# Kernel optimization log

Hardware: AMD Instinct MI355X
Metric: run time of the kernel (lower is better)

The kernel has to match this reference:

```python
import jax, jax.numpy as jnp
import numpy as np

N_NODES = 100000
N_EDGES = 1600000
IN_F, HID_F, OUT_F = 64, 64, 16


def setup_inputs() -> dict:
    key = jax.random.key(0)
    k_x, k_e, k_w1, k_w2 = jax.random.split(key, 4)
    x = jax.random.normal(k_x, (N_NODES, IN_F), dtype=jnp.float32)
    edge_index = jax.random.randint(k_e, (2, N_EDGES), 0, N_NODES, dtype=jnp.int64)
    # Glorot-ish init for the GCNConv linear weights; bias zeros (PyG default)
    W1 = jax.random.normal(k_w1, (IN_F, HID_F), dtype=jnp.float32) / np.sqrt(IN_F)
    b1 = jnp.zeros((HID_F,), dtype=jnp.float32)
    W2 = jax.random.normal(k_w2, (HID_F, OUT_F), dtype=jnp.float32) / np.sqrt(HID_F)
    b2 = jnp.zeros((OUT_F,), dtype=jnp.float32)
    return {"x": x, "edge_index": edge_index, "W1": W1, "b1": b1, "W2": W2, "b2": b2}


def reference(x, edge_index, W1, b1, W2, b2):
    N = x.shape[0]
    # GCNConv: add self-loops, symmetric normalization D^-1/2 A D^-1/2
    loop = jnp.arange(N, dtype=edge_index.dtype)
    src = jnp.concatenate([edge_index[0], loop])  # [E+N]
    dst = jnp.concatenate([edge_index[1], loop])  # [E+N]
    deg = jax.ops.segment_sum(jnp.ones_like(dst, dtype=x.dtype), dst, num_segments=N)
    dis = jax.lax.rsqrt(deg)  # deg >= 1 due to self-loops
    norm = dis[src] * dis[dst]  # [E+N]

    def gcn_conv(h, W, b):
        h = h @ W                                   # [N, d_out]
        msg = h[src] * norm[:, None]                # gather + scale  [E+N, d_out]
        agg = jax.ops.segment_sum(msg, dst, num_segments=N)  # scatter-add
        return agg + b

    h = jax.nn.relu(gcn_conv(x, W1, b1))
    h = gcn_conv(h, W2, b2)
    return jax.nn.log_softmax(h, axis=1)
```

## Files before the change

kernel.cpp:

```cpp
#include <hip/hip_runtime.h>
#include <hip/hip_bf16.h>
#include <hip/hip_fp16.h>


#define F1 64
#define F2 16
#define NBKT 256
#define BSH 512
#define NPB 256
#define SBD 1024
#define STG 9216

typedef _Float16 f16x8 __attribute__((ext_vector_type(8)));
typedef _Float16 f16x4 __attribute__((ext_vector_type(4)));
typedef float f32x2 __attribute__((ext_vector_type(2)));
typedef float f32x4 __attribute__((ext_vector_type(4)));
typedef float f32x8 __attribute__((ext_vector_type(8)));

__device__ inline f32x8 shfl_xor_f32x8(f32x8 v, int off) {
  f32x8 r;
#pragma unroll
  for (int k = 0; k < 8; ++k) r[k] = __shfl_xor(v[k], off);
  return r;
}
__device__ inline f32x4 shfl_xor_f32x4(f32x4 v, int off) {
  f32x4 r;
#pragma unroll
  for (int k = 0; k < 4; ++k) r[k] = __shfl_xor(v[k], off);
  return r;
}

__device__ inline void acc_fp8x8(f32x2* a, uint2 v) {
  a[0] += __builtin_amdgcn_cvt_pk_f32_fp8((int)v.x, false);
  a[1] += __builtin_amdgcn_cvt_pk_f32_fp8((int)v.x, true);
  a[2] += __builtin_amdgcn_cvt_pk_f32_fp8((int)v.y, false);
  a[3] += __builtin_amdgcn_cvt_pk_f32_fp8((int)v.y, true);
}

__global__ void k_w(const float* __restrict__ W1, const float* __restrict__ W2,
                    const float* __restrict__ b1,
                    __half* __restrict__ W1T, __half* __restrict__ W2Tp,
                    float* __restrict__ b1p, int* __restrict__ bcur, int nb) {
  int t = threadIdx.x;
  for (int i = t; i < 64 * 64; i += 256) {
    int n = i >> 6, k = i & 63;
    W1T[i] = __float2half(W1[k * 64 + n]);
  }
  for (int i = t; i < 16 * 64; i += 256) {
    int j = i >> 6, p = i & 63;
    int fp = 16 * (p & 3) + (p >> 2);
    W2Tp[i] = __float2half(W2[fp * 16 + j]);
  }
  if (t < 64) b1p[t] = b1[16 * (t & 3) + (t >> 2)];
  if (t < nb) bcur[t] = t * STG;
}

__global__ void k_bscatter(const int* __restrict__ src, const int* __restrict__ dst,
                           int* __restrict__ bcur, int* __restrict__ tmp,
                           int E, int nb, int chunk) {
  __shared__ int h[NBKT];
  __shared__ int cur[NBKT];
  int t = threadIdx.x, sb = blockIdx.x;
  int beg = sb * chunk, end = min(beg + chunk, E);
  if (t < NBKT) h[t] = 0;
  __syncthreads();
  int e;
  for (e = beg + t * 4; e + 4 <= end; e += 4 * SBD) {
    int4 d4 = *(const int4*)(dst + e);
    atomicAdd(&h[d4.x >> 9], 1);
    atomicAdd(&h[d4.y >> 9], 1);
    atomicAdd(&h[d4.z >> 9], 1);
    atomicAdd(&h[d4.w >> 9], 1);
  }
  for (; e < end; ++e) atomicAdd(&h[dst[e] >> 9], 1);
  __syncthreads();
  if (t < nb) cur[t] = atomicAdd(&bcur[t], h[t]);
  __syncthreads();
  for (e = beg + t * 4; e + 4 <= end; e += 4 * SBD) {
    int4 d4 = *(const int4*)(dst + e);
    int4 s4 = *(const int4*)(src + e);
    int b, off;
    b = d4.x >> 9; off = atomicAdd(&cur[b], 1); tmp[off] = (s4.x << 9) | (d4.x & 511);
    b = d4.y >> 9; off = atomicAdd(&cur[b], 1); tmp[off] = (s4.y << 9) | (d4.y & 511);
    b = d4.z >> 9; off = atomicAdd(&cur[b], 1); tmp[off] = (s4.z << 9) | (d4.z & 511);
    b = d4.w >> 9; off = atomicAdd(&cur[b], 1); tmp[off] = (s4.w << 9) | (d4.w & 511);
  }
  for (; e < end; ++e) {
    int d = dst[e];
    int b = d >> 9;
    int off = atomicAdd(&cur[b], 1);
    tmp[off] = (src[e] << 9) | (d & 511);
  }
}

__global__ void k_csr(const int* __restrict__ tmp, const int* __restrict__ bcur,
                      int* __restrict__ csr, int* __restrict__ rowptr,
                      float* __restrict__ dis, int N, int nb) {
  __shared__ int stage[STG];
  __shared__ int sc[BSH];
  __shared__ int cnt[BSH];
  __shared__ int lofs[BSH];
  int b = blockIdx.x, t = threadIdx.x;
  int lenb = bcur[b] - b * STG;
  if (t < NBKT) sc[t] = (t < nb) ? (bcur[t] - t * STG) : 0;
  __syncthreads();
  for (int off = 1; off < NBKT; off <<= 1) {
    int a = (t < NBKT && t >= off) ? sc[t - off] : 0;
    __syncthreads();
    if (t < NBKT) sc[t] += a;
    __syncthreads();
  }
  int beg = (b == 0) ? 0 : sc[b - 1];
  __syncthreads();
  int s0 = b * STG;
  int lim = lenb & ~3;
  for (int i = t * 4; i < lim; i += 4 * BSH)
    *(int4*)(stage + i) = *(const int4*)(tmp + s0 + i);
  {
    int r = lim + t;
    if (r < lenb) stage[r] = tmp[s0 + r];
  }
  cnt[t] = 0;
  __syncthreads();
  for (int i = t; i < lenb; i += BSH) atomicAdd(&cnt[stage[i] & (BSH - 1)], 1);
  __syncthreads();
  sc[t] = cnt[t];
  __syncthreads();
  for (int off = 1; off < BSH; off <<= 1) {
    int a = (t >= off) ? sc[t - off] : 0;
    __syncthreads();
    sc[t] += a;
    __syncthreads();
  }
  int excl = (t == 0) ? 0 : sc[t - 1];
  lofs[t] = excl;
  int n = b * BSH + t;
  if (n <= N) rowptr[n] = beg + excl;
  if (n < N) dis[n] = rsqrtf((float)(cnt[t] + 1));
  cnt[t] = 0;
  __syncthreads();
  for (int i = t; i < lenb; i += BSH) {
    int p = stage[i];
    int l = p & (BSH - 1);
    int off = atomicAdd(&cnt[l], 1);
    csr[beg + lofs[l] + off] = p >> 9;
  }
}

__global__ void k_gemm1(const float* __restrict__ x, const __half* __restrict__ W1T,
                        const float* __restrict__ dis, unsigned char* __restrict__ out,
                        int N) {
  int t = threadIdx.x;
  int wv = t >> 6, lane = t & 63;
  int m = lane & 15, q = lane >> 4;
  int row0 = blockIdx.x * 64 + wv * 16;
  int arow = min(row0 + m, N - 1);
  const _Float16* wt = (const _Float16*)W1T;
  f16x8 bf[4][2];
#pragma unroll
  for (int c = 0; c < 4; ++c)
#pragma unroll
    for (int kt = 0; kt < 2; ++kt)
      bf[c][kt] = *(const f16x8*)&wt[(c * 16 + m) * 64 + kt * 32 + q * 8];
  f16x8 a[2];
#pragma unroll
  for (int kt = 0; kt < 2; ++kt) {
    const float4* xp = (const float4*)(x + (size_t)arow * 64 + kt * 32 + q * 8);
    float4 u = xp[0], v = xp[1];
    a[kt][0] = (_Float16)u.x; a[kt][1] = (_Float16)u.y;
    a[kt][2] = (_Float16)u.z; a[kt][3] = (_Float16)u.w;
    a[kt][4] = (_Float16)v.x; a[kt][5] = (_Float16)v.y;
    a[kt][6] = (_Float16)v.z; a[kt][7] = (_Float16)v.w;
  }
  f32x4 acc[4] = {};
#pragma unroll
  for (int kt = 0; kt < 2; ++kt)
#pragma unroll
    for (int c = 0; c < 4; ++c)
      acc[c] = __builtin_amdgcn_mfma_f32_16x16x32_f16(a[kt], bf[c][kt], acc[c], 0, 0, 0);
#pragma unroll
  for (int r = 0; r < 4; ++r) {
    int n = row0 + q * 4 + r;
    if (n < N) {
      float dn = dis[n];
      int d = __builtin_amdgcn_cvt_pk_fp8_f32(acc[0][r] * dn, acc[1][r] * dn, 0, false);
      d = __builtin_amdgcn_cvt_pk_fp8_f32(acc[2][r] * dn, acc[3][r] * dn, d, true);
      *(unsigned int*)(out + (size_t)n * 64 + m * 4) = (unsigned)d;
    }
  }
}

__global__ void k_agg1f(const unsigned char* __restrict__ h, const float* __restrict__ dis,
                        const int* __restrict__ rowptr, const int* __restrict__ csr,
                        const float* __restrict__ b1p, const __half* __restrict__ W2Tp,
                        __half* __restrict__ h2, int N) {
  int gt = blockIdx.x * blockDim.x + threadIdx.x;
  int w = gt >> 6;
  int lane = gt & 63;
  int half = lane >> 5;
  int sub = (lane >> 3) & 3;
  int fl = lane & 7;
  int n = w * 2 + half;
  if (n >= N) return;
  float dn = dis[n];
  float4 bu = *(const float4*)(b1p + fl * 8);
  float4 bv = *(const float4*)(b1p + fl * 8 + 4);
  const _Float16* wt = (const _Float16*)W2Tp;
  f16x8 wj[4];
#pragma unroll
  for (int i = 0; i < 4; ++i)
    wj[i] = *(const f16x8*)&wt[(sub * 4 + i) * 64 + fl * 8];
  f32x2 a0[4] = {}, a1[4] = {};
  if (sub == 0)
    acc_fp8x8(a0, *(const uint2*)&h[(size_t)n * 64 + fl * 8]);
  int beg = rowptr[n], end = rowptr[n + 1];
  int e = beg + sub;
  int sA = (e < end) ? csr[e] : -1;
  int sB = (e + 4 < end) ? csr[e + 4] : -1;
  while (sB >= 0) {
    int e2 = e + 8;
    int sC = (e2 < end) ? csr[e2] : -1;
    int sD = (e2 + 4 < end) ? csr[e2 + 4] : -1;
    uint2 v0 = *(const uint2*)&h[(size_t)sA * 64 + fl * 8];
    uint2 v1 = *(const uint2*)&h[(size_t)sB * 64 + fl * 8];
    acc_fp8x8(a0, v0);
    acc_fp8x8(a1, v1);
    sA = sC; sB = sD; e = e2;
  }
  if (sA >= 0)
    acc_fp8x8(a0, *(const uint2*)&h[(size_t)sA * 64 + fl * 8]);
  f32x8 acc;
#pragma unroll
  for (int k = 0; k < 4; ++k) {
    f32x2 s = a0[k] + a1[k];
    acc[2 * k] = s[0];
    acc[2 * k + 1] = s[1];
  }
  acc += shfl_xor_f32x8(acc, 8);
  acc += shfl_xor_f32x8(acc, 16);
  float bb[8] = {bu.x, bu.y, bu.z, bu.w, bv.x, bv.y, bv.z, bv.w};
  float hr[8];
#pragma unroll
  for (int k = 0; k < 8; ++k)
    hr[k] = fmaxf(fmaf(dn, acc[k], bb[k]), 0.f);
  float p[4];
#pragma unroll
  for (int i = 0; i < 4; ++i) {
    float s = 0.f;
#pragma unroll
    for (int k = 0; k < 8; ++k) s = fmaf(hr[k], (float)wj[i][k], s);
    s += __shfl_xor(s, 1);
    s += __shfl_xor(s, 2);
    s += __shfl_xor(s, 4);
    p[i] = s;
  }
  if (fl == 0) {
    f16x4 o;
#pragma unroll
    for (int i = 0; i < 4; ++i) o[i] = (_Float16)(p[i] * dn);
    *(f16x4*)((_Float16*)h2 + (size_t)n * 16 + sub * 4) = o;
  }
}

__global__ void k_agg2(const __half* __restrict__ h2, const float* __restrict__ dis,
                       const int* __restrict__ rowptr, const int* __restrict__ csr,
                       const float* __restrict__ b2, float* __restrict__ out, int N) {
  int gt = blockIdx.x * blockDim.x + threadIdx.x;
  int w = gt >> 6;
  int lane = gt & 63;
  int half = lane >> 5;
  int sub = (lane >> 2) & 7;
  int fl = lane & 3;
  int n = w * 2 + half;
  if (n >= N) return;
  const _Float16* hp = (const _Float16*)h2;
  f32x4 acc0 = {}, acc1 = {};
  if (sub == 0)
    acc0 = __builtin_convertvector(*(const f16x4*)&hp[(size_t)n * 16 + fl * 4], f32x4);
  int beg = rowptr[n], end = rowptr[n + 1];
  int e = beg + sub;
  int sA = (e < end) ? csr[e] : -1;
  int sB = (e + 8 < end) ? csr[e + 8] : -1;
  while (sB >= 0) {
    int e2 = e + 16;
    int sC = (e2 < end) ? csr[e2] : -1;
    int sD = (e2 + 8 < end) ? csr[e2 + 8] : -1;
    f16x4 v0 = *(const f16x4*)&hp[(size_t)sA * 16 + fl * 4];
    f16x4 v1 = *(const f16x4*)&hp[(size_t)sB * 16 + fl * 4];
    acc0 += __builtin_convertvector(v0, f32x4);
    acc1 += __builtin_convertvector(v1, f32x4);
    sA = sC; sB = sD; e = e2;
  }
  if (sA >= 0)
    acc0 += __builtin_convertvector(*(const f16x4*)&hp[(size_t)sA * 16 + fl * 4], f32x4);
  f32x4 acc = acc0 + acc1;
  acc += shfl_xor_f32x4(acc, 4);
  acc += shfl_xor_f32x4(acc, 8);
  acc += shfl_xor_f32x4(acc, 16);
  if (sub == 0) {
    float dn = dis[n];
    float4 bb = *(const float4*)(b2 + fl * 4);
    float v0 = fmaf(dn, acc[0], bb.x);
    float v1 = fmaf(dn, acc[1], bb.y);
    float v2 = fmaf(dn, acc[2], bb.z);
    float v3 = fmaf(dn, acc[3], bb.w);
    float m = fmaxf(fmaxf(v0, v1), fmaxf(v2, v3));
    m = fmaxf(m, __shfl_xor(m, 1));
    m = fmaxf(m, __shfl_xor(m, 2));
    float s2 = __expf(v0 - m) + __expf(v1 - m) + __expf(v2 - m) + __expf(v3 - m);
    s2 += __shfl_xor(s2, 1);
    s2 += __shfl_xor(s2, 2);
    float ls = m + __logf(s2);
    float4 o = {v0 - ls, v1 - ls, v2 - ls, v3 - ls};
    *(float4*)(out + (size_t)n * 16 + fl * 4) = o;
  }
}

extern "C" void kernel_launch(void* const* d_in, const int* in_sizes, int n_in,
                              void* d_out, int out_size, void* d_ws, size_t ws_size,
                              hipStream_t stream) {
  const float* x = (const float*)d_in[0];
  const int* ei = (const int*)d_in[1];
  const float* W1 = (const float*)d_in[2];
  const float* b1 = (const float*)d_in[3];
  const float* W2 = (const float*)d_in[4];
  const float* b2 = (const float*)d_in[5];
  float* out = (float*)d_out;

  int N = in_sizes[0] / F1;
  int E = in_sizes[1] / 2;
  const int* src = ei;
  const int* dst = ei + E;
  int nb = (N + BSH - 1) >> 9;
  int chunk = ((E + NPB - 1) / NPB + 3) & ~3;

  char* ws = (char*)d_ws;
  size_t o_w1t = 0;
  size_t o_w2t = o_w1t + 64 * 64 * 2;
  size_t o_b1p = (o_w2t + 16 * 64 * 2 + 255) & ~(size_t)255;
  size_t o_bcur = (o_b1p + 64 * 4 + 255) & ~(size_t)255;
  size_t o_dis = (o_bcur + NBKT * 4 + 255) & ~(size_t)255;
  size_t o_rowp = (o_dis + (size_t)N * 4 + 255) & ~(size_t)255;
  size_t o_tmp = (o_rowp + (size_t)(N + 1) * 4 + 255) & ~(size_t)255;
  size_t o_csr = (o_tmp + (size_t)nb * STG * 4 + 255) & ~(size_t)255;
  size_t o_h1 = (o_csr + (size_t)E * 4 + 255) & ~(size_t)255;
  size_t o_h2 = (o_h1 + (size_t)N * 64 + 255) & ~(size_t)255;

  __half* W1T = (__half*)(ws + o_w1t);
  __half* W2Tp = (__half*)(ws + o_w2t);
  float* b1p = (float*)(ws + o_b1p);
  int* bcur = (int*)(ws + o_bcur);
  float* dis = (float*)(ws + o_dis);
  int* rowptr = (int*)(ws + o_rowp);
  int* tmp = (int*)(ws + o_tmp);
  int* csr = (int*)(ws + o_csr);
  unsigned char* h1 = (unsigned char*)(ws + o_h1);
  __half* h2 = (__half*)(ws + o_h2);

  k_w<<<1, 256, 0, stream>>>(W1, W2, b1, W1T, W2Tp, b1p, bcur, nb);
  k_bscatter<<<NPB, SBD, 0, stream>>>(src, dst, bcur, tmp, E, nb, chunk);
  k_csr<<<nb, BSH, 0, stream>>>(tmp, bcur, csr, rowptr, dis, N, nb);
  int gb = (N + 63) / 64;
  k_gemm1<<<gb, 256, 0, stream>>>(x, W1T, dis, h1, N);
  int aw = (N + 1) / 2;
  k_agg1f<<<((size_t)aw * 64 + 255) / 256, 256, 0, stream>>>(h1, dis, rowptr, csr, b1p, W2Tp, h2, N);
  k_agg2<<<((size_t)aw * 64 + 255) / 256, 256, 0, stream>>>(h2, dis, rowptr, csr, b2, out, N);
}
```

Before: 184.3 us.

## Fuse weight prep into bscatter, merge CSR build with GEMM1, deepen aggregation prefetch

The weight transpose/convert kernel becomes an extra block of the bucket-scatter kernel, and bucket cursors plus a new per-node degree array are zeroed by a memset. Degrees are counted with global atomics during scatter, so GEMM1 no longer waits on the CSR build and runs as extra blocks of the same launch, computing dis itself. Merging kernels cuts launch count and lets the CSR build and GEMM1 run concurrently. The layer-1 aggregation loop now prefetches four neighbor indices instead of two to raise memory-level parallelism. The cost is 1.6M extra global atomics on deg, with contention on popular nodes.

Result: slower. 251.2 us (+36.4%).

```diff
diff --git a/kernel.cpp b/kernel.cpp
--- a/kernel.cpp
+++ b/kernel.cpp
@@ -37,30 +37,29 @@
   a[3] += __builtin_amdgcn_cvt_pk_f32_fp8((int)v.y, true);
 }
 
-__global__ void k_w(const float* __restrict__ W1, const float* __restrict__ W2,
-                    const float* __restrict__ b1,
-                    __half* __restrict__ W1T, __half* __restrict__ W2Tp,
-                    float* __restrict__ b1p, int* __restrict__ bcur, int nb) {
-  int t = threadIdx.x;
-  for (int i = t; i < 64 * 64; i += 256) {
-    int n = i >> 6, k = i & 63;
-    W1T[i] = __float2half(W1[k * 64 + n]);
-  }
-  for (int i = t; i < 16 * 64; i += 256) {
-    int j = i >> 6, p = i & 63;
-    int fp = 16 * (p & 3) + (p >> 2);
-    W2Tp[i] = __float2half(W2[fp * 16 + j]);
-  }
-  if (t < 64) b1p[t] = b1[16 * (t & 3) + (t >> 2)];
-  if (t < nb) bcur[t] = t * STG;
-}
-
 __global__ void k_bscatter(const int* __restrict__ src, const int* __restrict__ dst,
                            int* __restrict__ bcur, int* __restrict__ tmp,
-                           int E, int nb, int chunk) {
+                           int* __restrict__ deg, int E, int nb, int chunk,
+                           const float* __restrict__ W1, const float* __restrict__ W2,
+                           const float* __restrict__ b1,
+                           __half* __restrict__ W1T, __half* __restrict__ W2Tp,
+                           float* __restrict__ b1p) {
+  int t = threadIdx.x, sb = blockIdx.x;
+  if (sb == NPB) {
+    for (int i = t; i < 64 * 64; i += SBD) {
+      int n = i >> 6, k = i & 63;
+      W1T[i] = __float2half(W1[k * 64 + n]);
+    }
+    for (int i = t; i < 16 * 64; i += SBD) {
+      int j = i >> 6, p = i & 63;
+      int fp = 16 * (p & 3) + (p >> 2);
+      W2Tp[i] = __float2half(W2[fp * 16 + j]);
+    }
+    if (t < 64) b1p[t] = b1[16 * (t & 3) + (t >> 2)];
+    return;
+  }
   __shared__ int h[NBKT];
   __shared__ int cur[NBKT];
-  int t = threadIdx.x, sb = blockIdx.x;
   int beg = sb * chunk, end = min(beg + chunk, E);
   if (t < NBKT) h[t] = 0;
   __syncthreads();
@@ -71,10 +70,18 @@
     atomicAdd(&h[d4.y >> 9], 1);
     atomicAdd(&h[d4.z >> 9], 1);
     atomicAdd(&h[d4.w >> 9], 1);
-  }
-  for (; e < end; ++e) atomicAdd(&h[dst[e] >> 9], 1);
-  __syncthreads();
-  if (t < nb) cur[t] = atomicAdd(&bcur[t], h[t]);
+    atomicAdd(&deg[d4.x], 1);
+    atomicAdd(&deg[d4.y], 1);
+    atomicAdd(&deg[d4.z], 1);
+    atomicAdd(&deg[d4.w], 1);
+  }
+  for (; e < end; ++e) {
+    int d = dst[e];
+    atomicAdd(&h[d >> 9], 1);
+    atomicAdd(&deg[d], 1);
+  }
+  __syncthreads();
+  if (t < nb) cur[t] = t * STG + atomicAdd(&bcur[t], h[t]);
   __syncthreads();
   for (e = beg + t * 4; e + 4 <= end; e += 4 * SBD) {
     int4 d4 = *(const int4*)(dst + e);
@@ -93,16 +100,60 @@
   }
 }
 
-__global__ void k_csr(const int* __restrict__ tmp, const int* __restrict__ bcur,
-                      int* __restrict__ csr, int* __restrict__ rowptr,
-                      float* __restrict__ dis, int N, int nb) {
+__global__ void k_cg(const int* __restrict__ tmp, const int* __restrict__ bcur,
+                     int* __restrict__ csr, int* __restrict__ rowptr,
+                     const float* __restrict__ x, const __half* __restrict__ W1T,
+                     const int* __restrict__ deg, float* __restrict__ dis,
+                     unsigned char* __restrict__ h1, int N, int nb) {
   __shared__ int stage[STG];
   __shared__ int sc[BSH];
   __shared__ int cnt[BSH];
   __shared__ int lofs[BSH];
   int b = blockIdx.x, t = threadIdx.x;
-  int lenb = bcur[b] - b * STG;
-  if (t < NBKT) sc[t] = (t < nb) ? (bcur[t] - t * STG) : 0;
+  if (b >= nb) {
+    int g = b - nb;
+    int wv = t >> 6, lane = t & 63;
+    int m = lane & 15, q = lane >> 4;
+    int row0 = g * 128 + wv * 16;
+    int arow = min(row0 + m, N - 1);
+    const _Float16* wt = (const _Float16*)W1T;
+    f16x8 bf[4][2];
+#pragma unroll
+    for (int c = 0; c < 4; ++c)
+#pragma unroll
+      for (int kt = 0; kt < 2; ++kt)
+        bf[c][kt] = *(const f16x8*)&wt[(c * 16 + m) * 64 + kt * 32 + q * 8];
+    f16x8 a[2];
+#pragma unroll
+    for (int kt = 0; kt < 2; ++kt) {
+      const float4* xp = (const float4*)(x + (size_t)arow * 64 + kt * 32 + q * 8);
+      float4 u = xp[0], v = xp[1];
+      a[kt][0] = (_Float16)u.x; a[kt][1] = (_Float16)u.y;
+      a[kt][2] = (_Float16)u.z; a[kt][3] = (_Float16)u.w;
+      a[kt][4] = (_Float16)v.x; a[kt][5] = (_Float16)v.y;
+      a[kt][6] = (_Float16)v.z; a[kt][7] = (_Float16)v.w;
+    }
+    f32x4 acc[4] = {};
+#pragma unroll
+    for (int kt = 0; kt < 2; ++kt)
+#pragma unroll
+      for (int c = 0; c < 4; ++c)
+        acc[c] = __builtin_amdgcn_mfma_f32_16x16x32_f16(a[kt], bf[c][kt], acc[c], 0, 0, 0);
+#pragma unroll
+    for (int r = 0; r < 4; ++r) {
+      int n = row0 + q * 4 + r;
+      if (n < N) {
+        float dn = rsqrtf((float)(deg[n] + 1));
+        if (m == 0) dis[n] = dn;
+        int d = __builtin_amdgcn_cvt_pk_fp8_f32(acc[0][r] * dn, acc[1][r] * dn, 0, false);
+        d = __builtin_amdgcn_cvt_pk_fp8_f32(acc[2][r] * dn, acc[3][r] * dn, d, true);
+        *(unsigned int*)(h1 + (size_t)n * 64 + m * 4) = (unsigned)d;
+      }
+    }
+    return;
+  }
+  int lenb = bcur[b];
+  if (t < NBKT) sc[t] = (t < nb) ? bcur[t] : 0;
   __syncthreads();
   for (int off = 1; off < NBKT; off <<= 1) {
     int a = (t < NBKT && t >= off) ? sc[t - off] : 0;
@@ -136,7 +187,6 @@
   lofs[t] = excl;
   int n = b * BSH + t;
   if (n <= N) rowptr[n] = beg + excl;
-  if (n < N) dis[n] = rsqrtf((float)(cnt[t] + 1));
   cnt[t] = 0;
   __syncthreads();
   for (int i = t; i < lenb; i += BSH) {
@@ -144,49 +194,6 @@
     int l = p & (BSH - 1);
     int off = atomicAdd(&cnt[l], 1);
     csr[beg + lofs[l] + off] = p >> 9;
-  }
-}
-
-__global__ void k_gemm1(const float* __restrict__ x, const __half* __restrict__ W1T,
-                        const float* __restrict__ dis, unsigned char* __restrict__ out,
-                        int N) {
-  int t = threadIdx.x;
-  int wv = t >> 6, lane = t & 63;
-  int m = lane & 15, q = lane >> 4;
-  int row0 = blockIdx.x * 64 + wv * 16;
-  int arow = min(row0 + m, N - 1);
-  const _Float16* wt = (const _Float16*)W1T;
-  f16x8 bf[4][2];
-#pragma unroll
-  for (int c = 0; c < 4; ++c)
-#pragma unroll
-    for (int kt = 0; kt < 2; ++kt)
-      bf[c][kt] = *(const f16x8*)&wt[(c * 16 + m) * 64 + kt * 32 + q * 8];
-  f16x8 a[2];
-#pragma unroll
-  for (int kt = 0; kt < 2; ++kt) {
-    const float4* xp = (const float4*)(x + (size_t)arow * 64 + kt * 32 + q * 8);
-    float4 u = xp[0], v = xp[1];
-    a[kt][0] = (_Float16)u.x; a[kt][1] = (_Float16)u.y;
-    a[kt][2] = (_Float16)u.z; a[kt][3] = (_Float16)u.w;
-    a[kt][4] = (_Float16)v.x; a[kt][5] = (_Float16)v.y;
-    a[kt][6] = (_Float16)v.z; a[kt][7] = (_Float16)v.w;
-  }
-  f32x4 acc[4] = {};
-#pragma unroll
-  for (int kt = 0; kt < 2; ++kt)
-#pragma unroll
-    for (int c = 0; c < 4; ++c)
-      acc[c] = __builtin_amdgcn_mfma_f32_16x16x32_f16(a[kt], bf[c][kt], acc[c], 0, 0, 0);
-#pragma unroll
-  for (int r = 0; r < 4; ++r) {
-    int n = row0 + q * 4 + r;
-    if (n < N) {
-      float dn = dis[n];
-      int d = __builtin_amdgcn_cvt_pk_fp8_f32(acc[0][r] * dn, acc[1][r] * dn, 0, false);
-      d = __builtin_amdgcn_cvt_pk_fp8_f32(acc[2][r] * dn, acc[3][r] * dn, d, true);
-      *(unsigned int*)(out + (size_t)n * 64 + m * 4) = (unsigned)d;
-    }
   }
 }
 
@@ -215,20 +222,29 @@
     acc_fp8x8(a0, *(const uint2*)&h[(size_t)n * 64 + fl * 8]);
   int beg = rowptr[n], end = rowptr[n + 1];
   int e = beg + sub;
-  int sA = (e < end) ? csr[e] : -1;
-  int sB = (e + 4 < end) ? csr[e + 4] : -1;
-  while (sB >= 0) {
-    int e2 = e + 8;
-    int sC = (e2 < end) ? csr[e2] : -1;
-    int sD = (e2 + 4 < end) ? csr[e2 + 4] : -1;
-    uint2 v0 = *(const uint2*)&h[(size_t)sA * 64 + fl * 8];
-    uint2 v1 = *(const uint2*)&h[(size_t)sB * 64 + fl * 8];
+  int s0 = (e < end) ? csr[e] : -1;
+  int s1 = (e + 4 < end) ? csr[e + 4] : -1;
+  int s2 = (e + 8 < end) ? csr[e + 8] : -1;
+  int s3 = (e + 12 < end) ? csr[e + 12] : -1;
+  while (s3 >= 0) {
+    int e2 = e + 16;
+    int t0 = (e2 < end) ? csr[e2] : -1;
+    int t1 = (e2 + 4 < end) ? csr[e2 + 4] : -1;
+    int t2 = (e2 + 8 < end) ? csr[e2 + 8] : -1;
+    int t3 = (e2 + 12 < end) ? csr[e2 + 12] : -1;
+    uint2 v0 = *(const uint2*)&h[(size_t)s0 * 64 + fl * 8];
+    uint2 v1 = *(const uint2*)&h[(size_t)s1 * 64 + fl * 8];
+    uint2 v2 = *(const uint2*)&h[(size_t)s2 * 64 + fl * 8];
+    uint2 v3 = *(const uint2*)&h[(size_t)s3 * 64 + fl * 8];
     acc_fp8x8(a0, v0);
     acc_fp8x8(a1, v1);
-    sA = sC; sB = sD; e = e2;
-  }
-  if (sA >= 0)
-    acc_fp8x8(a0, *(const uint2*)&h[(size_t)sA * 64 + fl * 8]);
+    acc_fp8x8(a0, v2);
+    acc_fp8x8(a1, v3);
+    s0 = t0; s1 = t1; s2 = t2; s3 = t3; e = e2;
+  }
+  if (s0 >= 0) acc_fp8x8(a0, *(const uint2*)&h[(size_t)s0 * 64 + fl * 8]);
+  if (s1 >= 0) acc_fp8x8(a1, *(const uint2*)&h[(size_t)s1 * 64 + fl * 8]);
+  if (s2 >= 0) acc_fp8x8(a0, *(const uint2*)&h[(size_t)s2 * 64 + fl * 8]);
   f32x8 acc;
 #pragma unroll
   for (int k = 0; k < 4; ++k) {
@@ -339,7 +355,8 @@
   size_t o_w2t = o_w1t + 64 * 64 * 2;
   size_t o_b1p = (o_w2t + 16 * 64 * 2 + 255) & ~(size_t)255;
   size_t o_bcur = (o_b1p + 64 * 4 + 255) & ~(size_t)255;
-  size_t o_dis = (o_bcur + NBKT * 4 + 255) & ~(size_t)255;
+  size_t o_deg = (o_bcur + NBKT * 4 + 255) & ~(size_t)255;
+  size_t o_dis = (o_deg + (size_t)N * 4 + 255) & ~(size_t)255;
   size_t o_rowp = (o_dis + (size_t)N * 4 + 255) & ~(size_t)255;
   size_t o_tmp = (o_rowp + (size_t)(N + 1) * 4 + 255) & ~(size_t)255;
   size_t o_csr = (o_tmp + (size_t)nb * STG * 4 + 255) & ~(size_t)255;
@@ -350,6 +367,7 @@
   __half* W2Tp = (__half*)(ws + o_w2t);
   float* b1p = (float*)(ws + o_b1p);
   int* bcur = (int*)(ws + o_bcur);
+  int* deg = (int*)(ws + o_deg);
   float* dis = (float*)(ws + o_dis);
   int* rowptr = (int*)(ws + o_rowp);
   int* tmp = (int*)(ws + o_tmp);
@@ -357,11 +375,12 @@
   unsigned char* h1 = (unsigned char*)(ws + o_h1);
   __half* h2 = (__half*)(ws + o_h2);
 
-  k_w<<<1, 256, 0, stream>>>(W1, W2, b1, W1T, W2Tp, b1p, bcur, nb);
-  k_bscatter<<<NPB, SBD, 0, stream>>>(src, dst, bcur, tmp, E, nb, chunk);
-  k_csr<<<nb, BSH, 0, stream>>>(tmp, bcur, csr, rowptr, dis, N, nb);
-  int gb = (N + 63) / 64;
-  k_gemm1<<<gb, 256, 0, stream>>>(x, W1T, dis, h1, N);
+  hipMemsetAsync(bcur, 0, (o_deg - o_bcur) + (size_t)N * 4, stream);
+  k_bscatter<<<NPB + 1, SBD, 0, stream>>>(src, dst, bcur, tmp, deg, E, nb, chunk,
+                                          W1, W2, b1, W1T, W2Tp, b1p);
+  int gb2 = (N + 127) / 128;
+  k_cg<<<nb + gb2, BSH, 0, stream>>>(tmp, bcur, csr, rowptr, x, W1T, deg, dis,
+                                     h1, N, nb);
   int aw = (N + 1) / 2;
   k_agg1f<<<((size_t)aw * 64 + 255) / 256, 256, 0, stream>>>(h1, dis, rowptr, csr, b1p, W2Tp, h2, N);
   k_agg2<<<((size_t)aw * 64 + 255) / 256, 256, 0, stream>>>(h2, dis, rowptr, csr, b2, out, N);
```

## Fuse first-layer GEMM into CSR build kernel using shared degree normalization

Applied to the files above, without the earlier changes.

Merges the CSR construction kernel and the first GEMM into one kernel. Each 512-thread block builds CSR rows for its 512-node bucket, keeps the inverse sqrt degrees in shared memory, then its 8 waves each compute 64 rows of x@W1 with MFMA and write fp8 output. This removes one kernel launch and the global re-read of dis. In exchange the GEMM now runs on only ~196 blocks with serial per-wave iterations, which lowers parallelism and may hurt latency hiding for the x loads.

New measurement: 182.9 us. No clear change (-0.7%).

```diff
diff --git a/kernel.cpp b/kernel.cpp
--- a/kernel.cpp
+++ b/kernel.cpp
@@ -93,13 +93,16 @@
   }
 }
 
-__global__ void k_csr(const int* __restrict__ tmp, const int* __restrict__ bcur,
+__global__ void k_cg2(const int* __restrict__ tmp, const int* __restrict__ bcur,
                       int* __restrict__ csr, int* __restrict__ rowptr,
-                      float* __restrict__ dis, int N, int nb) {
+                      float* __restrict__ dis,
+                      const float* __restrict__ x, const __half* __restrict__ W1T,
+                      unsigned char* __restrict__ h1, int N, int nb) {
   __shared__ int stage[STG];
   __shared__ int sc[BSH];
   __shared__ int cnt[BSH];
   __shared__ int lofs[BSH];
+  __shared__ float dnode[BSH];
   int b = blockIdx.x, t = threadIdx.x;
   int lenb = bcur[b] - b * STG;
   if (t < NBKT) sc[t] = (t < nb) ? (bcur[t] - t * STG) : 0;
@@ -135,8 +138,10 @@
   int excl = (t == 0) ? 0 : sc[t - 1];
   lofs[t] = excl;
   int n = b * BSH + t;
+  float dn_t = rsqrtf((float)(cnt[t] + 1));
+  dnode[t] = dn_t;
   if (n <= N) rowptr[n] = beg + excl;
-  if (n < N) dis[n] = rsqrtf((float)(cnt[t] + 1));
+  if (n < N) dis[n] = dn_t;
   cnt[t] = 0;
   __syncthreads();
   for (int i = t; i < lenb; i += BSH) {
@@ -145,16 +150,8 @@
     int off = atomicAdd(&cnt[l], 1);
     csr[beg + lofs[l] + off] = p >> 9;
   }
-}
-
-__global__ void k_gemm1(const float* __restrict__ x, const __half* __restrict__ W1T,
-                        const float* __restrict__ dis, unsigned char* __restrict__ out,
-                        int N) {
-  int t = threadIdx.x;
   int wv = t >> 6, lane = t & 63;
   int m = lane & 15, q = lane >> 4;
-  int row0 = blockIdx.x * 64 + wv * 16;
-  int arow = min(row0 + m, N - 1);
   const _Float16* wt = (const _Float16*)W1T;
   f16x8 bf[4][2];
 #pragma unroll
@@ -162,30 +159,37 @@
 #pragma unroll
     for (int kt = 0; kt < 2; ++kt)
       bf[c][kt] = *(const f16x8*)&wt[(c * 16 + m) * 64 + kt * 32 + q * 8];
-  f16x8 a[2];
-#pragma unroll
-  for (int kt = 0; kt < 2; ++kt) {
-    const float4* xp = (const float4*)(x + (size_t)arow * 64 + kt * 32 + q * 8);
-    float4 u = xp[0], v = xp[1];
-    a[kt][0] = (_Float16)u.x; a[kt][1] = (_Float16)u.y;
-    a[kt][2] = (_Float16)u.z; a[kt][3] = (_Float16)u.w;
-    a[kt][4] = (_Float16)v.x; a[kt][5] = (_Float16)v.y;
-    a[kt][6] = (_Float16)v.z; a[kt][7] = (_Float16)v.w;
-  }
-  f32x4 acc[4] = {};
-#pragma unroll
-  for (int kt = 0; kt < 2; ++kt)
-#pragma unroll
-    for (int c = 0; c < 4; ++c)
-      acc[c] = __builtin_amdgcn_mfma_f32_16x16x32_f16(a[kt], bf[c][kt], acc[c], 0, 0, 0);
-#pragma unroll
-  for (int r = 0; r < 4; ++r) {
-    int n = row0 + q * 4 + r;
-    if (n < N) {
-      float dn = dis[n];
-      int d = __builtin_amdgcn_cvt_pk_fp8_f32(acc[0][r] * dn, acc[1][r] * dn, 0, false);
-      d = __builtin_amdgcn_cvt_pk_fp8_f32(acc[2][r] * dn, acc[3][r] * dn, d, true);
-      *(unsigned int*)(out + (size_t)n * 64 + m * 4) = (unsigned)d;
+#pragma unroll
+  for (int it = 0; it < 4; ++it) {
+    int lrow0 = wv * 64 + it * 16;
+    int row0 = b * BSH + lrow0;
+    int arow = min(row0 + m, N - 1);
+    f16x8 a[2];
+#pragma unroll
+    for (int kt = 0; kt < 2; ++kt) {
+      const float4* xp = (const float4*)(x + (size_t)arow * 64 + kt * 32 + q * 8);
+      float4 u = xp[0], v = xp[1];
+      a[kt][0] = (_Float16)u.x; a[kt][1] = (_Float16)u.y;
+      a[kt][2] = (_Float16)u.z; a[kt][3] = (_Float16)u.w;
+      a[kt][4] = (_Float16)v.x; a[kt][5] = (_Float16)v.y;
+      a[kt][6] = (_Float16)v.z; a[kt][7] = (_Float16)v.w;
+    }
+    f32x4 acc[4] = {};
+#pragma unroll
+    for (int kt = 0; kt < 2; ++kt)
+#pragma unroll
+      for (int c = 0; c < 4; ++c)
+        acc[c] = __builtin_amdgcn_mfma_f32_16x16x32_f16(a[kt], bf[c][kt], acc[c], 0, 0, 0);
+#pragma unroll
+    for (int r = 0; r < 4; ++r) {
+      int lr = lrow0 + q * 4 + r;
+      int nn = b * BSH + lr;
+      if (nn < N) {
+        float dn = dnode[lr];
+        int d = __builtin_amdgcn_cvt_pk_fp8_f32(acc[0][r] * dn, acc[1][r] * dn, 0, false);
+        d = __builtin_amdgcn_cvt_pk_fp8_f32(acc[2][r] * dn, acc[3][r] * dn, d, true);
+        *(unsigned int*)(h1 + (size_t)nn * 64 + m * 4) = (unsigned)d;
+      }
     }
   }
 }
@@ -359,9 +363,7 @@
 
   k_w<<<1, 256, 0, stream>>>(W1, W2, b1, W1T, W2Tp, b1p, bcur, nb);
   k_bscatter<<<NPB, SBD, 0, stream>>>(src, dst, bcur, tmp, E, nb, chunk);
-  k_csr<<<nb, BSH, 0, stream>>>(tmp, bcur, csr, rowptr, dis, N, nb);
-  int gb = (N + 63) / 64;
-  k_gemm1<<<gb, 256, 0, stream>>>(x, W1T, dis, h1, N);
+  k_cg2<<<nb, BSH, 0, stream>>>(tmp, bcur, csr, rowptr, dis, x, W1T, h1, N, nb);
   int aw = (N + 1) / 2;
   k_agg1f<<<((size_t)aw * 64 + 255) / 256, 256, 0, stream>>>(h1, dis, rowptr, csr, b1p, W2Tp, h2, N);
   k_agg2<<<((size_t)aw * 64 + 255) / 256, 256, 0, stream>>>(h2, dis, rowptr, csr, b2, out, N);
```
